# Optimization experiments

Measured on AMD Instinct MI355X. Metric: run time of the kernel, lower is better.

## Reference

```python
import jax, jax.numpy as jnp
import numpy as np

S, B = 64, 256
CH_IN, CH_OUT, AUX, HID = 128, 128, 3, 32
EPS = 1e-5


def _ln(h, g, b):
    mu = jnp.mean(h, axis=-1, keepdims=True)
    var = jnp.mean(jnp.square(h - mu), axis=-1, keepdims=True)
    return (h - mu) * jax.lax.rsqrt(var + EPS) * g + b


def _hyper_mlp(z, W1, b1, g1, be1, W2, b2, g2, be2, W3, b3):
    # Linear -> LN -> ReLU -> Linear -> LN -> ReLU -> Linear (droprate=0)
    h = jax.nn.relu(_ln(jnp.einsum('sba,ha->sbh', z, W1) + b1, g1, be1))
    h = jax.nn.relu(_ln(jnp.einsum('sbh,kh->sbk', h, W2) + b2, g2, be2))
    return jnp.einsum('sbh,oh->sbo', h, W3) + b3


def setup_inputs() -> dict:
    key = jax.random.key(0)
    ks = jax.random.split(key, 24)
    f = lambda k, shp: (jax.random.normal(k, shp, dtype=jnp.float32) * 0.05)
    inp = {
        'x': jax.random.normal(ks[0], (S, B, CH_IN), dtype=jnp.float32),
        'z': jax.random.normal(ks[1], (S, B, AUX), dtype=jnp.float32),
        # weight-branch hypernet params
        'wW1': f(ks[2], (HID, AUX)), 'wb1': jnp.zeros((HID,), jnp.float32),
        'wg1': jnp.ones((HID,), jnp.float32), 'wbe1': jnp.zeros((HID,), jnp.float32),
        'wW2': f(ks[3], (HID, HID)), 'wb2': jnp.zeros((HID,), jnp.float32),
        'wg2': jnp.ones((HID,), jnp.float32), 'wbe2': jnp.zeros((HID,), jnp.float32),
        'wW3': f(ks[4], (CH_OUT * CH_IN, HID)), 'wb3': jnp.zeros((CH_OUT * CH_IN,), jnp.float32),
        # bias-branch hypernet params
        'bW1': f(ks[5], (HID, AUX)), 'bb1': jnp.zeros((HID,), jnp.float32),
        'bg1': jnp.ones((HID,), jnp.float32), 'bbe1': jnp.zeros((HID,), jnp.float32),
        'bW2': f(ks[6], (HID, HID)), 'bb2': jnp.zeros((HID,), jnp.float32),
        'bg2': jnp.ones((HID,), jnp.float32), 'bbe2': jnp.zeros((HID,), jnp.float32),
        'bW3': f(ks[7], (CH_OUT, HID)), 'bb3': jnp.zeros((CH_OUT,), jnp.float32),
    }
    return inp


def reference(x, z,
              wW1, wb1, wg1, wbe1, wW2, wb2, wg2, wbe2, wW3, wb3,
              bW1, bb1, bg1, bbe1, bW2, bb2, bg2, bbe2, bW3, bb3):
    # per-token weight: [S,B,ch_out*ch_in] -> [S,B,ch_out,ch_in]
    weight = _hyper_mlp(z, wW1, wb1, wg1, wbe1, wW2, wb2, wg2, wbe2, wW3, wb3)
    weight = weight.reshape(S, B, CH_OUT, CH_IN)
    bias = _hyper_mlp(z, bW1, bb1, bg1, bbe1, bW2, bb2, bg2, bbe2, bW3, bb3)
    # batched mat-vec: out[s,b,o] = sum_i weight[s,b,o,i] * x[s,b,i] + bias
    out = jnp.einsum('sboi,sbi->sbo', weight, x) + bias
    return out
```

## Files before the change

### kernel.cpp

```cpp
#include <hip/hip_runtime.h>
#include <hip/hip_bf16.h>
#include <stdint.h>

#define T_DIM   16384
#define KR      4288
#define NT      67
#define LN_EPS  1e-5f

typedef __attribute__((ext_vector_type(8))) short  short8;
typedef __attribute__((ext_vector_type(4))) float  f32x4;
typedef __attribute__((ext_vector_type(8))) __bf16 bf8;

__device__ __forceinline__ void g2l16(const ushort* g, ushort* l) {
  __builtin_amdgcn_global_load_lds(
      (const __attribute__((address_space(1))) uint32_t*)g,
      (__attribute__((address_space(3))) uint32_t*)l, 16, 0, 0);
}

__global__ __launch_bounds__(256) void prep_w3(
    const float* __restrict__ wW3, const float* __restrict__ wb3,
    const float* __restrict__ bW3, ushort* __restrict__ w3b)
{
  const int cid = blockIdx.x * 256 + threadIdx.x;
  const int o   = blockIdx.y;
  if (cid >= KR / 8) return;
  const int k0    = cid * 8;
  const int slice = k0 >> 5;
  const int q     = (k0 >> 3) & 3;
  const int pcc   = q ^ ((o >> 1) & 3);
  float v[8];
  if (slice < 132) {
    const float* src = (slice < 128)
        ? wW3 + ((size_t)o * 128 + slice) * 32 + pcc * 8
        : wb3 + (size_t)o * 128 + (slice - 128) * 32 + pcc * 8;
    float4 a = *(const float4*)src;
    float4 b = *(const float4*)(src + 4);
    v[0]=a.x; v[1]=a.y; v[2]=a.z; v[3]=a.w; v[4]=b.x; v[5]=b.y; v[6]=b.z; v[7]=b.w;
  } else if (slice == 132) {
    const float* src = bW3 + (size_t)o * 32 + pcc * 8;
    float4 a = *(const float4*)src;
    float4 b = *(const float4*)(src + 4);
    v[0]=a.x; v[1]=a.y; v[2]=a.z; v[3]=a.w; v[4]=b.x; v[5]=b.y; v[6]=b.z; v[7]=b.w;
  } else {
#pragma unroll
    for (int j = 0; j < 8; ++j) v[j] = 0.f;
  }
  bf8 pk;
#pragma unroll
  for (int j = 0; j < 8; ++j) pk[j] = (__bf16)v[j];
  *(short8*)(w3b + (size_t)o * KR + k0) = *(short8*)&pk;
}

__global__ __launch_bounds__(256) void fused_kernel(
    const float* __restrict__ x, const float* __restrict__ z,
    const float* __restrict__ wW1, const float* __restrict__ wb1,
    const float* __restrict__ wg1, const float* __restrict__ wbe1,
    const float* __restrict__ wW2, const float* __restrict__ wb2,
    const float* __restrict__ wg2, const float* __restrict__ wbe2,
    const float* __restrict__ bW1, const float* __restrict__ bb1,
    const float* __restrict__ bg1, const float* __restrict__ bbe1,
    const float* __restrict__ bW2, const float* __restrict__ bb2,
    const float* __restrict__ bg2, const float* __restrict__ bbe2,
    const float* __restrict__ bb3,
    const ushort* __restrict__ w3b, float* __restrict__ out)
{
  __shared__ __align__(16) ushort xs[64][136];
  __shared__ __align__(16) ushort bsm[3][4096];
  __shared__ __align__(16) float  h2w_s[64][36];
  __shared__ __align__(16) ushort h2b_s[64][40];

  const int tid  = threadIdx.x;
  const int lane = tid & 63;
  const int wid  = tid >> 6;
  const int wr   = wid >> 1, wc = wid & 1;
  const int lm   = lane & 15, hc = lane >> 4, hbase = hc * 8;
  const int t0   = (blockIdx.x >> 1) * 64;
  const int o0   = (blockIdx.x & 1) * 64;

  const int idx0 = tid, idx1 = tid + 256;
  const ushort* sp0 = w3b + (size_t)(o0 + ((idx0 >> 2) & 63)) * KR
                          + (idx0 >> 8) * 32 + (idx0 & 3) * 8;
  const ushort* sp1 = w3b + (size_t)(o0 + ((idx1 >> 2) & 63)) * KR
                          + (idx1 >> 8) * 32 + (idx1 & 3) * 8;
  auto stage = [&](int buf) {
    g2l16(sp0, &bsm[buf][idx0 * 8]);
    g2l16(sp1, &bsm[buf][idx1 * 8]);
    sp0 += 64; sp1 += 64;
  };

  stage(0);
  stage(1);

  float bb3v[2];
#pragma unroll
  for (int n = 0; n < 2; ++n) bb3v[n] = bb3[o0 + wc * 32 + n * 16 + lm];

  {
    const int r = tid >> 2, q = tid & 3;
    const float* src = x + (size_t)(t0 + r) * 128 + q * 32;
#pragma unroll
    for (int u = 0; u < 8; ++u) {
      float4 v = *(const float4*)(src + u * 4);
      __bf16 c0 = (__bf16)v.x, c1 = (__bf16)v.y, c2 = (__bf16)v.z, c3 = (__bf16)v.w;
      ushort4 w;
      w.x = *(ushort*)&c0; w.y = *(ushort*)&c1; w.z = *(ushort*)&c2; w.w = *(ushort*)&c3;
      *(ushort4*)&xs[r][q * 32 + u * 4] = w;
    }
  }

  if (tid < 128) {
    const int br  = tid >> 6;
    const int row = tid & 63;
    const int tok = t0 + row;
    const float* W1  = br ? bW1  : wW1;  const float* b1  = br ? bb1  : wb1;
    const float* g1  = br ? bg1  : wg1;  const float* be1 = br ? bbe1 : wbe1;
    const float* W2  = br ? bW2  : wW2;  const float* b2  = br ? bb2  : wb2;
    const float* g2  = br ? bg2  : wg2;  const float* be2 = br ? bbe2 : wbe2;

    const float z0 = z[tok * 3 + 0], z1 = z[tok * 3 + 1], z2 = z[tok * 3 + 2];

    float h1[32];
    float s = 0.f, s2 = 0.f;
#pragma unroll
    for (int j = 0; j < 32; ++j) {
      float v = W1[j * 3] * z0 + W1[j * 3 + 1] * z1 + W1[j * 3 + 2] * z2 + b1[j];
      h1[j] = v; s += v; s2 += v * v;
    }
    float mu  = s * (1.f / 32.f);
    float var = fmaxf(s2 * (1.f / 32.f) - mu * mu, 0.f);
    float rr  = rsqrtf(var + LN_EPS);
#pragma unroll
    for (int j = 0; j < 32; ++j)
      h1[j] = fmaxf((h1[j] - mu) * rr * g1[j] + be1[j], 0.f);

    float h2a[32];
    s = 0.f; s2 = 0.f;
#pragma unroll
    for (int j = 0; j < 32; ++j) {
      float acc = b2[j];
#pragma unroll
      for (int kk = 0; kk < 8; ++kk) {
        float4 w = *(const float4*)&W2[j * 32 + kk * 4];
        acc += w.x * h1[kk * 4] + w.y * h1[kk * 4 + 1]
             + w.z * h1[kk * 4 + 2] + w.w * h1[kk * 4 + 3];
      }
      h2a[j] = acc; s += acc; s2 += acc * acc;
    }
    mu  = s * (1.f / 32.f);
    var = fmaxf(s2 * (1.f / 32.f) - mu * mu, 0.f);
    rr  = rsqrtf(var + LN_EPS);
    if (br == 0) {
#pragma unroll
      for (int j4 = 0; j4 < 8; ++j4) {
        float4 w;
        w.x = fmaxf((h2a[j4*4+0] - mu) * rr * g2[j4*4+0] + be2[j4*4+0], 0.f);
        w.y = fmaxf((h2a[j4*4+1] - mu) * rr * g2[j4*4+1] + be2[j4*4+1], 0.f);
        w.z = fmaxf((h2a[j4*4+2] - mu) * rr * g2[j4*4+2] + be2[j4*4+2], 0.f);
        w.w = fmaxf((h2a[j4*4+3] - mu) * rr * g2[j4*4+3] + be2[j4*4+3], 0.f);
        *(float4*)&h2w_s[row][j4 * 4] = w;
      }
    } else {
#pragma unroll
      for (int j8 = 0; j8 < 4; ++j8) {
        bf8 pk;
#pragma unroll
        for (int j = 0; j < 8; ++j)
          pk[j] = (__bf16)fmaxf((h2a[j8*8+j] - mu) * rr * g2[j8*8+j] + be2[j8*8+j], 0.f);
        *(short8*)&h2b_s[row][j8 * 8] = *(short8*)&pk;
      }
    }
  }

  __syncthreads();

  int rl[2];
  rl[0] = wr * 32 + lm;
  rl[1] = wr * 32 + 16 + lm;

  float h2f[2][8];
  short8 h2bf[2];
#pragma unroll
  for (int m = 0; m < 2; ++m) {
    float4 a = *(const float4*)&h2w_s[rl[m]][hbase];
    float4 c = *(const float4*)&h2w_s[rl[m]][hbase + 4];
    h2f[m][0]=a.x; h2f[m][1]=a.y; h2f[m][2]=a.z; h2f[m][3]=a.w;
    h2f[m][4]=c.x; h2f[m][5]=c.y; h2f[m][6]=c.z; h2f[m][7]=c.w;
    h2bf[m] = *(const short8*)&h2b_s[rl[m]][hbase];
  }

  int boffs[2][2];
#pragma unroll
  for (int n = 0; n < 2; ++n) {
    int ol  = wc * 32 + n * 16 + lm;
    int chc = hc ^ ((ol >> 1) & 3);
#pragma unroll
    for (int i2 = 0; i2 < 2; ++i2)
      boffs[i2][n] = i2 * 2048 + ol * 32 + chc * 8;
  }

  f32x4 acc[2][2];
#pragma unroll
  for (int m = 0; m < 2; ++m)
#pragma unroll
    for (int n = 0; n < 2; ++n) acc[m][n] = (f32x4){0.f, 0.f, 0.f, 0.f};

  int cur = 0;
#pragma unroll 1
  for (int ks = 0; ks < NT; ++ks) {
    if (ks < NT - 1) asm volatile("s_waitcnt vmcnt(2)" ::: "memory");
    else             asm volatile("s_waitcnt vmcnt(0)" ::: "memory");
    __builtin_amdgcn_s_barrier();
    asm volatile("" ::: "memory");

    if (ks + 2 < NT) {
      int sb = cur + 2; if (sb >= 3) sb -= 3;
      stage(sb);
    }

    short8 af[2][2];
    if (ks < 64) {
#pragma unroll
      for (int m = 0; m < 2; ++m) {
        uint32_t xp = *(const uint32_t*)&xs[rl[m]][2 * ks];
        union { uint32_t u; float f; } lo, hi;
        lo.u = xp << 16;
        hi.u = xp & 0xffff0000u;
        bf8 a0, a1;
#pragma unroll
        for (int jj = 0; jj < 8; ++jj) {
          a0[jj] = (__bf16)(lo.f * h2f[m][jj]);
          a1[jj] = (__bf16)(hi.f * h2f[m][jj]);
        }
        af[0][m] = *(short8*)&a0;
        af[1][m] = *(short8*)&a1;
      }
    } else if (ks < 66) {
#pragma unroll
      for (int i2 = 0; i2 < 2; ++i2) {
        int s = (ks - 64) * 2 + i2;
#pragma unroll
        for (int m = 0; m < 2; ++m)
          af[i2][m] = *(const short8*)&xs[rl[m]][s * 32 + hbase];
      }
    } else {
#pragma unroll
      for (int m = 0; m < 2; ++m) { af[0][m] = h2bf[m]; af[1][m] = h2bf[m]; }
    }

#pragma unroll
    for (int i2 = 0; i2 < 2; ++i2) {
#pragma unroll
      for (int n = 0; n < 2; ++n) {
        short8 bfr = *(const short8*)&bsm[cur][boffs[i2][n]];
#pragma unroll
        for (int m = 0; m < 2; ++m)
          acc[m][n] = __builtin_amdgcn_mfma_f32_16x16x32_bf16(
              af[i2][m], bfr, acc[m][n], 0, 0, 0);
      }
    }

    cur = (cur == 2) ? 0 : cur + 1;
  }

#pragma unroll
  for (int m = 0; m < 2; ++m) {
    const int gr0 = t0 + wr * 32 + m * 16 + hc * 4;
#pragma unroll
    for (int n = 0; n < 2; ++n) {
      const int gc = o0 + wc * 32 + n * 16 + lm;
#pragma unroll
      for (int r_ = 0; r_ < 4; ++r_) {
        const int row = gr0 + r_;
        out[(size_t)row * 128 + gc] = acc[m][n][r_] + bb3v[n];
      }
    }
  }
}

extern "C" void kernel_launch(void* const* d_in, const int* in_sizes, int n_in,
                              void* d_out, int out_size, void* d_ws, size_t ws_size,
                              hipStream_t stream)
{
  const float* x    = (const float*)d_in[0];
  const float* z    = (const float*)d_in[1];
  const float* wW1  = (const float*)d_in[2];
  const float* wb1  = (const float*)d_in[3];
  const float* wg1  = (const float*)d_in[4];
  const float* wbe1 = (const float*)d_in[5];
  const float* wW2  = (const float*)d_in[6];
  const float* wb2  = (const float*)d_in[7];
  const float* wg2  = (const float*)d_in[8];
  const float* wbe2 = (const float*)d_in[9];
  const float* wW3  = (const float*)d_in[10];
  const float* wb3  = (const float*)d_in[11];
  const float* bW1  = (const float*)d_in[12];
  const float* bb1  = (const float*)d_in[13];
  const float* bg1  = (const float*)d_in[14];
  const float* bbe1 = (const float*)d_in[15];
  const float* bW2  = (const float*)d_in[16];
  const float* bb2  = (const float*)d_in[17];
  const float* bg2  = (const float*)d_in[18];
  const float* bbe2 = (const float*)d_in[19];
  const float* bW3  = (const float*)d_in[20];
  const float* bb3  = (const float*)d_in[21];

  ushort* w3b = (ushort*)d_ws;
  float*  outf = (float*)d_out;

  hipLaunchKernelGGL(prep_w3, dim3(3, 128), dim3(256), 0, stream,
                     wW3, wb3, bW3, w3b);
  hipLaunchKernelGGL(fused_kernel, dim3(512), dim3(256), 0, stream,
                     x, z,
                     wW1, wb1, wg1, wbe1, wW2, wb2, wg2, wbe2,
                     bW1, bb1, bg1, bbe1, bW2, bb2, bg2, bbe2,
                     bb3, w3b, outf);
}
```

Before: 60.44 us.

## Switch to fp16 MFMA with split-K across blocks and direct-global B loads

The main GEMM moves from bf16 to fp16 MFMA, and the x·h2 A-fragment products are computed with packed half2 multiplies instead of fp32 multiplies followed by bf16 conversion. Work is now split along the K dimension across block pairs: each block covers all 128 outputs for 64 tokens over half the K range. Results are combined with atomicAdd into an output that is zeroed by a memset first. The LDS triple-buffer staging and per-step barriers are gone; each wave loads its B fragments straight from global memory into registers with double buffering. This trades barrier and LDS cost for float atomics, which make the sum order nondeterministic, an extra memset, and fp16 range and precision risk.

Result: slower. 63.39 us (+4.9%).

```diff
diff --git a/kernel.cpp b/kernel.cpp
--- a/kernel.cpp
+++ b/kernel.cpp
@@ -1,43 +1,35 @@
 #include <hip/hip_runtime.h>
-#include <hip/hip_bf16.h>
+#include <hip/hip_fp16.h>
 #include <stdint.h>
 
-#define T_DIM   16384
 #define KR      4288
-#define NT      67
 #define LN_EPS  1e-5f
 
-typedef __attribute__((ext_vector_type(8))) short  short8;
-typedef __attribute__((ext_vector_type(4))) float  f32x4;
-typedef __attribute__((ext_vector_type(8))) __bf16 bf8;
-
-__device__ __forceinline__ void g2l16(const ushort* g, ushort* l) {
-  __builtin_amdgcn_global_load_lds(
-      (const __attribute__((address_space(1))) uint32_t*)g,
-      (__attribute__((address_space(3))) uint32_t*)l, 16, 0, 0);
-}
+typedef _Float16 f16;
+typedef __attribute__((ext_vector_type(2))) _Float16 h2v;
+typedef __attribute__((ext_vector_type(4))) _Float16 h4v;
+typedef __attribute__((ext_vector_type(8))) _Float16 h8v;
+typedef __attribute__((ext_vector_type(4))) float    f32x4;
+
+union H2U { uint32_t u; h2v h; };
+union H8U { uint32_t u[4]; h8v v; };
 
 __global__ __launch_bounds__(256) void prep_w3(
     const float* __restrict__ wW3, const float* __restrict__ wb3,
-    const float* __restrict__ bW3, ushort* __restrict__ w3b)
+    const float* __restrict__ bW3, f16* __restrict__ w3h)
 {
   const int cid = blockIdx.x * 256 + threadIdx.x;
   const int o   = blockIdx.y;
   if (cid >= KR / 8) return;
   const int k0    = cid * 8;
   const int slice = k0 >> 5;
-  const int q     = (k0 >> 3) & 3;
-  const int pcc   = q ^ ((o >> 1) & 3);
+  const int h0    = k0 & 31;
   float v[8];
-  if (slice < 132) {
-    const float* src = (slice < 128)
-        ? wW3 + ((size_t)o * 128 + slice) * 32 + pcc * 8
-        : wb3 + (size_t)o * 128 + (slice - 128) * 32 + pcc * 8;
-    float4 a = *(const float4*)src;
-    float4 b = *(const float4*)(src + 4);
-    v[0]=a.x; v[1]=a.y; v[2]=a.z; v[3]=a.w; v[4]=b.x; v[5]=b.y; v[6]=b.z; v[7]=b.w;
-  } else if (slice == 132) {
-    const float* src = bW3 + (size_t)o * 32 + pcc * 8;
+  if (slice < 133) {
+    const float* src;
+    if      (slice < 128) src = wW3 + ((size_t)o * 128 + slice) * 32 + h0;
+    else if (slice < 132) src = wb3 + (size_t)o * 128 + (slice - 128) * 32 + h0;
+    else                  src = bW3 + (size_t)o * 32 + h0;
     float4 a = *(const float4*)src;
     float4 b = *(const float4*)(src + 4);
     v[0]=a.x; v[1]=a.y; v[2]=a.z; v[3]=a.w; v[4]=b.x; v[5]=b.y; v[6]=b.z; v[7]=b.w;
@@ -45,10 +37,10 @@
 #pragma unroll
     for (int j = 0; j < 8; ++j) v[j] = 0.f;
   }
-  bf8 pk;
-#pragma unroll
-  for (int j = 0; j < 8; ++j) pk[j] = (__bf16)v[j];
-  *(short8*)(w3b + (size_t)o * KR + k0) = *(short8*)&pk;
+  h8v pk;
+#pragma unroll
+  for (int j = 0; j < 8; ++j) pk[j] = (f16)v[j];
+  *(h8v*)(w3h + (size_t)o * KR + k0) = pk;
 }
 
 __global__ __launch_bounds__(256) void fused_kernel(
@@ -62,38 +54,26 @@
     const float* __restrict__ bW2, const float* __restrict__ bb2,
     const float* __restrict__ bg2, const float* __restrict__ bbe2,
     const float* __restrict__ bb3,
-    const ushort* __restrict__ w3b, float* __restrict__ out)
+    const f16* __restrict__ w3h, float* __restrict__ out)
 {
-  __shared__ __align__(16) ushort xs[64][136];
-  __shared__ __align__(16) ushort bsm[3][4096];
-  __shared__ __align__(16) float  h2w_s[64][36];
-  __shared__ __align__(16) ushort h2b_s[64][40];
+  __shared__ __align__(16) f16 xs[64][136];
+  __shared__ __align__(16) f16 h2w_s[64][40];
+  __shared__ __align__(16) f16 h2b_s[64][40];
 
   const int tid  = threadIdx.x;
   const int lane = tid & 63;
   const int wid  = tid >> 6;
-  const int wr   = wid >> 1, wc = wid & 1;
   const int lm   = lane & 15, hc = lane >> 4, hbase = hc * 8;
-  const int t0   = (blockIdx.x >> 1) * 64;
-  const int o0   = (blockIdx.x & 1) * 64;
-
-  const int idx0 = tid, idx1 = tid + 256;
-  const ushort* sp0 = w3b + (size_t)(o0 + ((idx0 >> 2) & 63)) * KR
-                          + (idx0 >> 8) * 32 + (idx0 & 3) * 8;
-  const ushort* sp1 = w3b + (size_t)(o0 + ((idx1 >> 2) & 63)) * KR
-                          + (idx1 >> 8) * 32 + (idx1 & 3) * 8;
-  auto stage = [&](int buf) {
-    g2l16(sp0, &bsm[buf][idx0 * 8]);
-    g2l16(sp1, &bsm[buf][idx1 * 8]);
-    sp0 += 64; sp1 += 64;
-  };
-
-  stage(0);
-  stage(1);
-
-  float bb3v[2];
-#pragma unroll
-  for (int n = 0; n < 2; ++n) bb3v[n] = bb3[o0 + wc * 32 + n * 16 + lm];
+  const int tile = blockIdx.x >> 1;
+  const int kh   = blockIdx.x & 1;
+  const int t0   = tile * 64;
+  const int o0   = wid * 32;
+  const int ks0    = kh * 34;
+  const int n_iter = kh ? 33 : 34;
+
+  float bbv[2];
+#pragma unroll
+  for (int n = 0; n < 2; ++n) bbv[n] = bb3[o0 + n * 16 + lm] * (float)kh;
 
   {
     const int r = tid >> 2, q = tid & 3;
@@ -101,10 +81,8 @@
 #pragma unroll
     for (int u = 0; u < 8; ++u) {
       float4 v = *(const float4*)(src + u * 4);
-      __bf16 c0 = (__bf16)v.x, c1 = (__bf16)v.y, c2 = (__bf16)v.z, c3 = (__bf16)v.w;
-      ushort4 w;
-      w.x = *(ushort*)&c0; w.y = *(ushort*)&c1; w.z = *(ushort*)&c2; w.w = *(ushort*)&c3;
-      *(ushort4*)&xs[r][q * 32 + u * 4] = w;
+      h4v p; p[0] = (f16)v.x; p[1] = (f16)v.y; p[2] = (f16)v.z; p[3] = (f16)v.w;
+      *(h4v*)&xs[r][q * 32 + u * 4] = p;
     }
   }
 
@@ -149,132 +127,118 @@
     mu  = s * (1.f / 32.f);
     var = fmaxf(s2 * (1.f / 32.f) - mu * mu, 0.f);
     rr  = rsqrtf(var + LN_EPS);
-    if (br == 0) {
-#pragma unroll
-      for (int j4 = 0; j4 < 8; ++j4) {
-        float4 w;
-        w.x = fmaxf((h2a[j4*4+0] - mu) * rr * g2[j4*4+0] + be2[j4*4+0], 0.f);
-        w.y = fmaxf((h2a[j4*4+1] - mu) * rr * g2[j4*4+1] + be2[j4*4+1], 0.f);
-        w.z = fmaxf((h2a[j4*4+2] - mu) * rr * g2[j4*4+2] + be2[j4*4+2], 0.f);
-        w.w = fmaxf((h2a[j4*4+3] - mu) * rr * g2[j4*4+3] + be2[j4*4+3], 0.f);
-        *(float4*)&h2w_s[row][j4 * 4] = w;
+    f16* dst = br ? &h2b_s[row][0] : &h2w_s[row][0];
+#pragma unroll
+    for (int j4 = 0; j4 < 8; ++j4) {
+      h4v w;
+      w[0] = (f16)fmaxf((h2a[j4*4+0] - mu) * rr * g2[j4*4+0] + be2[j4*4+0], 0.f);
+      w[1] = (f16)fmaxf((h2a[j4*4+1] - mu) * rr * g2[j4*4+1] + be2[j4*4+1], 0.f);
+      w[2] = (f16)fmaxf((h2a[j4*4+2] - mu) * rr * g2[j4*4+2] + be2[j4*4+2], 0.f);
+      w[3] = (f16)fmaxf((h2a[j4*4+3] - mu) * rr * g2[j4*4+3] + be2[j4*4+3], 0.f);
+      *(h4v*)&dst[j4 * 4] = w;
+    }
+  }
+
+  __syncthreads();
+
+  uint32_t h2p[4][4];
+#pragma unroll
+  for (int m = 0; m < 4; ++m) {
+    H8U c; c.v = *(const h8v*)&h2w_s[m * 16 + lm][hbase];
+#pragma unroll
+    for (int q = 0; q < 4; ++q) h2p[m][q] = c.u[q];
+  }
+
+  const f16* bp00 = w3h + (size_t)(o0 + lm)      * KR + (ks0 * 2    ) * 32 + hbase;
+  const f16* bp01 = w3h + (size_t)(o0 + 16 + lm) * KR + (ks0 * 2    ) * 32 + hbase;
+  const f16* bp10 = w3h + (size_t)(o0 + lm)      * KR + (ks0 * 2 + 1) * 32 + hbase;
+  const f16* bp11 = w3h + (size_t)(o0 + 16 + lm) * KR + (ks0 * 2 + 1) * 32 + hbase;
+
+#define LOADSET(S) do { \
+    S[0][0] = *(const h8v*)bp00; bp00 += 64; \
+    S[0][1] = *(const h8v*)bp01; bp01 += 64; \
+    S[1][0] = *(const h8v*)bp10; bp10 += 64; \
+    S[1][1] = *(const h8v*)bp11; bp11 += 64; } while (0)
+
+  f32x4 acc[4][2];
+#pragma unroll
+  for (int m = 0; m < 4; ++m)
+#pragma unroll
+    for (int n = 0; n < 2; ++n) acc[m][n] = (f32x4){0.f, 0.f, 0.f, 0.f};
+
+  auto STEP = [&](h8v (&bs)[2][2], int ks) {
+    const int ksg = ks0 + ks;
+    h8v af0[4], af1[4];
+    if (ksg < 64) {
+#pragma unroll
+      for (int m = 0; m < 4; ++m) {
+        const uint32_t xp = *(const uint32_t*)&xs[m * 16 + lm][2 * ksg];
+        H2U x0, x1;
+        x0.u = (xp & 0xffffu) | (xp << 16);
+        x1.u = (xp >> 16) | (xp & 0xffff0000u);
+        H8U r0, r1;
+#pragma unroll
+        for (int q = 0; q < 4; ++q) {
+          H2U hq; hq.u = h2p[m][q];
+          H2U p0; p0.h = x0.h * hq.h; r0.u[q] = p0.u;
+          H2U p1; p1.h = x1.h * hq.h; r1.u[q] = p1.u;
+        }
+        af0[m] = r0.v; af1[m] = r1.v;
+      }
+    } else if (ksg < 66) {
+      const int s = (ksg - 64) * 2;
+#pragma unroll
+      for (int m = 0; m < 4; ++m) {
+        af0[m] = *(const h8v*)&xs[m * 16 + lm][s * 32 + hbase];
+        af1[m] = *(const h8v*)&xs[m * 16 + lm][(s + 1) * 32 + hbase];
       }
     } else {
 #pragma unroll
-      for (int j8 = 0; j8 < 4; ++j8) {
-        bf8 pk;
-#pragma unroll
-        for (int j = 0; j < 8; ++j)
-          pk[j] = (__bf16)fmaxf((h2a[j8*8+j] - mu) * rr * g2[j8*8+j] + be2[j8*8+j], 0.f);
-        *(short8*)&h2b_s[row][j8 * 8] = *(short8*)&pk;
-      }
-    }
-  }
-
-  __syncthreads();
-
-  int rl[2];
-  rl[0] = wr * 32 + lm;
-  rl[1] = wr * 32 + 16 + lm;
-
-  float h2f[2][8];
-  short8 h2bf[2];
-#pragma unroll
-  for (int m = 0; m < 2; ++m) {
-    float4 a = *(const float4*)&h2w_s[rl[m]][hbase];
-    float4 c = *(const float4*)&h2w_s[rl[m]][hbase + 4];
-    h2f[m][0]=a.x; h2f[m][1]=a.y; h2f[m][2]=a.z; h2f[m][3]=a.w;
-    h2f[m][4]=c.x; h2f[m][5]=c.y; h2f[m][6]=c.z; h2f[m][7]=c.w;
-    h2bf[m] = *(const short8*)&h2b_s[rl[m]][hbase];
-  }
-
-  int boffs[2][2];
-#pragma unroll
-  for (int n = 0; n < 2; ++n) {
-    int ol  = wc * 32 + n * 16 + lm;
-    int chc = hc ^ ((ol >> 1) & 3);
-#pragma unroll
-    for (int i2 = 0; i2 < 2; ++i2)
-      boffs[i2][n] = i2 * 2048 + ol * 32 + chc * 8;
-  }
-
-  f32x4 acc[2][2];
-#pragma unroll
-  for (int m = 0; m < 2; ++m)
-#pragma unroll
-    for (int n = 0; n < 2; ++n) acc[m][n] = (f32x4){0.f, 0.f, 0.f, 0.f};
-
-  int cur = 0;
+      for (int m = 0; m < 4; ++m) {
+        af0[m] = *(const h8v*)&h2b_s[m * 16 + lm][hbase];
+        af1[m] = af0[m];
+      }
+    }
+#pragma unroll
+    for (int n = 0; n < 2; ++n)
+#pragma unroll
+      for (int m = 0; m < 4; ++m)
+        acc[m][n] = __builtin_amdgcn_mfma_f32_16x16x32_f16(af0[m], bs[0][n], acc[m][n], 0, 0, 0);
+#pragma unroll
+    for (int n = 0; n < 2; ++n)
+#pragma unroll
+      for (int m = 0; m < 4; ++m)
+        acc[m][n] = __builtin_amdgcn_mfma_f32_16x16x32_f16(af1[m], bs[1][n], acc[m][n], 0, 0, 0);
+  };
+
+  h8v bA[2][2], bB[2][2];
+  LOADSET(bA);
+  LOADSET(bB);
+
+  int ks = 0;
 #pragma unroll 1
-  for (int ks = 0; ks < NT; ++ks) {
-    if (ks < NT - 1) asm volatile("s_waitcnt vmcnt(2)" ::: "memory");
-    else             asm volatile("s_waitcnt vmcnt(0)" ::: "memory");
-    __builtin_amdgcn_s_barrier();
-    asm volatile("" ::: "memory");
-
-    if (ks + 2 < NT) {
-      int sb = cur + 2; if (sb >= 3) sb -= 3;
-      stage(sb);
-    }
-
-    short8 af[2][2];
-    if (ks < 64) {
-#pragma unroll
-      for (int m = 0; m < 2; ++m) {
-        uint32_t xp = *(const uint32_t*)&xs[rl[m]][2 * ks];
-        union { uint32_t u; float f; } lo, hi;
-        lo.u = xp << 16;
-        hi.u = xp & 0xffff0000u;
-        bf8 a0, a1;
-#pragma unroll
-        for (int jj = 0; jj < 8; ++jj) {
-          a0[jj] = (__bf16)(lo.f * h2f[m][jj]);
-          a1[jj] = (__bf16)(hi.f * h2f[m][jj]);
-        }
-        af[0][m] = *(short8*)&a0;
-        af[1][m] = *(short8*)&a1;
-      }
-    } else if (ks < 66) {
-#pragma unroll
-      for (int i2 = 0; i2 < 2; ++i2) {
-        int s = (ks - 64) * 2 + i2;
-#pragma unroll
-        for (int m = 0; m < 2; ++m)
-          af[i2][m] = *(const short8*)&xs[rl[m]][s * 32 + hbase];
-      }
-    } else {
-#pragma unroll
-      for (int m = 0; m < 2; ++m) { af[0][m] = h2bf[m]; af[1][m] = h2bf[m]; }
-    }
-
-#pragma unroll
-    for (int i2 = 0; i2 < 2; ++i2) {
-#pragma unroll
-      for (int n = 0; n < 2; ++n) {
-        short8 bfr = *(const short8*)&bsm[cur][boffs[i2][n]];
-#pragma unroll
-        for (int m = 0; m < 2; ++m)
-          acc[m][n] = __builtin_amdgcn_mfma_f32_16x16x32_bf16(
-              af[i2][m], bfr, acc[m][n], 0, 0, 0);
-      }
-    }
-
-    cur = (cur == 2) ? 0 : cur + 1;
-  }
-
-#pragma unroll
-  for (int m = 0; m < 2; ++m) {
-    const int gr0 = t0 + wr * 32 + m * 16 + hc * 4;
+  while (ks + 2 <= n_iter) {
+    STEP(bA, ks);
+    if (ks + 2 < n_iter) LOADSET(bA);
+    STEP(bB, ks + 1);
+    if (ks + 3 < n_iter) LOADSET(bB);
+    ks += 2;
+  }
+  if (ks < n_iter) STEP(bA, ks);
+
+#pragma unroll
+  for (int m = 0; m < 4; ++m) {
 #pragma unroll
     for (int n = 0; n < 2; ++n) {
-      const int gc = o0 + wc * 32 + n * 16 + lm;
+      const int gc = o0 + n * 16 + lm;
 #pragma unroll
       for (int r_ = 0; r_ < 4; ++r_) {
-        const int row = gr0 + r_;
-        out[(size_t)row * 128 + gc] = acc[m][n][r_] + bb3v[n];
-      }
-    }
-  }
+        const int row = t0 + m * 16 + hc * 4 + r_;
+        atomicAdd(&out[(size_t)row * 128 + gc], acc[m][n][r_] + bbv[n]);
+      }
+    }
+  }
+#undef LOADSET
 }
 
 extern "C" void kernel_launch(void* const* d_in, const int* in_sizes, int n_in,
@@ -304,14 +268,15 @@
   const float* bW3  = (const float*)d_in[20];
   const float* bb3  = (const float*)d_in[21];
 
-  ushort* w3b = (ushort*)d_ws;
-  float*  outf = (float*)d_out;
-
+  f16*   w3h  = (f16*)d_ws;
+  float* outf = (float*)d_out;
+
+  hipMemsetAsync(d_out, 0, (size_t)16384 * 128 * sizeof(float), stream);
   hipLaunchKernelGGL(prep_w3, dim3(3, 128), dim3(256), 0, stream,
-                     wW3, wb3, bW3, w3b);
+                     wW3, wb3, bW3, w3h);
   hipLaunchKernelGGL(fused_kernel, dim3(512), dim3(256), 0, stream,
                      x, z,
                      wW1, wb1, wg1, wbe1, wW2, wb2, wg2, wbe2,
                      bW1, bb1, bg1, bbe1, bW2, bb2, bg2, bbe2,
-                     bb3, w3b, outf);
+                     bb3, w3h, outf);
 }
```
